# Kernel tuning notes

Hardware: AMD Instinct MI355X
Metric: run time of the kernel (lower is better)

Reference implementation:

```python
import jax, jax.numpy as jnp
import numpy as np
import math

NEG_INF = -1000000000.0
D_EMBED = 1024
D_K = 1024
N_HEADS = 16
D_H = D_EMBED // N_HEADS


def setup_inputs() -> dict:
    key = jax.random.key(0)
    ks = jax.random.split(key, 12)
    B, S = 2, 2048
    s = 0.02
    return {
        "embed": jax.random.normal(ks[0], (B, S, D_EMBED), dtype=jnp.float32),
        "key": jax.random.normal(ks[1], (B, S, D_K), dtype=jnp.float32),
        "attn_mask": jax.random.randint(ks[2], (B, S, S), 0, 2, dtype=jnp.int32),
        "Wq": jax.random.normal(ks[3], (D_EMBED, D_EMBED), dtype=jnp.float32) * s,
        "bq": jnp.zeros((D_EMBED,), dtype=jnp.float32),
        "Wk": jax.random.normal(ks[4], (D_EMBED, D_K), dtype=jnp.float32) * s,
        "bk": jnp.zeros((D_EMBED,), dtype=jnp.float32),
        "Wv": jax.random.normal(ks[5], (D_EMBED, D_K), dtype=jnp.float32) * s,
        "bv": jnp.zeros((D_EMBED,), dtype=jnp.float32),
        "Wo": jax.random.normal(ks[6], (D_EMBED, D_EMBED), dtype=jnp.float32) * s,
        "bo": jnp.zeros((D_EMBED,), dtype=jnp.float32),
    }


def _alibi_bias(seq_len: int, n_heads: int) -> jnp.ndarray:
    # symmetric |i-j| distances, slopes 2^-(8k/H) for k=1..H
    r = jnp.arange(seq_len)
    pos = jnp.abs(r[None, :] - r[:, None]).astype(jnp.float32)  # [S, S]
    step = 8.0 / n_heads
    ms = 2.0 ** (-jnp.arange(step, 8.0 + step, step, dtype=jnp.float32))  # [H]
    return ms[:, None, None] * pos[None, :, :]  # [H, S, S]


def reference(embed, key, attn_mask, Wq, bq, Wk, bk, Wv, bv, Wo, bo):
    B, Sq, _ = embed.shape
    Sk = key.shape[1]
    Q = embed @ Wq.T + bq          # [B, Sq, D]
    K = key @ Wk.T + bk            # [B, Sk, D]
    V = key @ Wv.T + bv            # [B, Sk, D]
    Qh = Q.reshape(B, Sq, N_HEADS, D_H).transpose(0, 2, 1, 3)  # [B, H, Sq, d_h]
    Kh = K.reshape(B, Sk, N_HEADS, D_H).transpose(0, 2, 1, 3)
    Vh = V.reshape(B, Sk, N_HEADS, D_H).transpose(0, 2, 1, 3)
    attn = jnp.einsum("bhqd,bhkd->bhqk", Qh, Kh)
    # ALiBi bias subtracted BEFORE scaling (as in source)
    attn = attn - _alibi_bias(Sq, N_HEADS)[None]
    attn = attn * (1.0 / math.sqrt(D_EMBED))  # note: scale uses d_embed, not d_h
    attn = jnp.where(attn_mask[:, None, :, :] == 0, NEG_INF, attn)
    attn = jax.nn.softmax(attn, axis=-1)
    out = jnp.einsum("bhqk,bhkd->bhqd", attn, Vh)
    out = out.transpose(0, 2, 1, 3).reshape(B, Sq, D_EMBED)
    return out @ Wo.T + bo
```

## Files before the change

### kernel.cpp

```cpp
#include <hip/hip_runtime.h>


typedef _Float16 f16;
typedef __attribute__((ext_vector_type(8))) _Float16 f16x8;
typedef __attribute__((ext_vector_type(4))) _Float16 f16x4;
typedef __attribute__((ext_vector_type(4))) float f32x4;
typedef unsigned long long u64;
typedef unsigned int u32;

#define MFMA16 __builtin_amdgcn_mfma_f32_16x16x32_f16
#define MFMA16K16 __builtin_amdgcn_mfma_f32_16x16x16f16

__device__ __forceinline__ void gl16(const f16* g, f16* l) {
    __builtin_amdgcn_global_load_lds(
        (const __attribute__((address_space(1))) void*)(const void*)g,
        (__attribute__((address_space(3))) void*)(void*)l,
        16, 0, 0);
}

__global__ __launch_bounds__(256) void k_convert(
    const float* __restrict__ embed, const float* __restrict__ key,
    const float* __restrict__ wq, const float* __restrict__ wk,
    const float* __restrict__ wv, const float* __restrict__ wo,
    f16* __restrict__ xe, f16* __restrict__ xk,
    f16* __restrict__ wqh, f16* __restrict__ wkh,
    f16* __restrict__ wvh, f16* __restrict__ woh)
{
    long g = (long)blockIdx.x * 256 + threadIdx.x;
    const float* src; f16* dst; long off;
    if (g < 524288)       { src = embed; dst = xe; off = g; }
    else if (g < 1048576) { src = key;   dst = xk; off = g - 524288; }
    else {
        long t = g - 1048576; int wi = (int)(t >> 17); off = t & 131071;
        if (wi == 0)      { src = wq; dst = wqh; }
        else if (wi == 1) { src = wk; dst = wkh; }
        else if (wi == 2) { src = wv; dst = wvh; }
        else              { src = wo; dst = woh; }
    }
    const float4* s4 = (const float4*)src;
    float4 a = s4[off * 2], b = s4[off * 2 + 1];
    f16x8 o;
    o[0]=(f16)a.x; o[1]=(f16)a.y; o[2]=(f16)a.z; o[3]=(f16)a.w;
    o[4]=(f16)b.x; o[5]=(f16)b.y; o[6]=(f16)b.z; o[7]=(f16)b.w;
    *(f16x8*)(dst + off * 8) = o;
}

__global__ __launch_bounds__(256) void k_packmask(
    const int* __restrict__ mask, u64* __restrict__ bits)
{
    int gw = (blockIdx.x * 256 + threadIdx.x) >> 6;
    int lane = threadIdx.x & 63;
    const int* row = mask + (long)gw * 2048;
    u64* out = bits + (long)gw * 32;
    #pragma unroll 4
    for (int c = 0; c < 32; ++c) {
        int v = row[c * 64 + lane];
        u64 b = __ballot(v != 0);
        if (lane == 0) out[c] = b;
    }
}

__global__ __launch_bounds__(256) void k_qkv(
    const f16* __restrict__ xe, const f16* __restrict__ xk,
    const f16* __restrict__ wqh, const f16* __restrict__ wkh, const f16* __restrict__ wvh,
    const float* __restrict__ bq, const float* __restrict__ bk, const float* __restrict__ bv,
    f16* __restrict__ Qh, f16* __restrict__ Kh, f16* __restrict__ Vt)
{
    int bid = blockIdx.x;
    int which = bid >> 8;
    int rr_ = bid & 255;
    int tm = rr_ >> 3, tn = rr_ & 7;
    const f16* X = (which == 0) ? xe : xk;
    const f16* W = (which == 0) ? wqh : (which == 1) ? wkh : wvh;
    const float* bias = (which == 0) ? bq : (which == 1) ? bk : bv;

    __shared__ f16 smem[128 * 136];
    f16* la = smem;
    f16* lb = smem + 128 * 64;

    int tid = threadIdx.x;
    int lane = tid & 63, wid = tid >> 6;
    int wr = wid >> 1, wc = wid & 1;
    int lm = lane & 15, qd = lane >> 4;

    f32x4 acc[4][4];
    #pragma unroll
    for (int i = 0; i < 4; i++)
        #pragma unroll
        for (int j = 0; j < 4; j++) acc[i][j] = (f32x4)0.0f;

    int m0 = tm * 128, n0 = tn * 128;

    for (int kt = 0; kt < 16; ++kt) {
        int k0 = kt * 64;
        __syncthreads();
        #pragma unroll
        for (int t = 0; t < 4; ++t) {
            int cid = tid + t * 256;
            int row = cid >> 3;
            int cg = cid & 7;
            int sw = cg ^ (row & 7);
            *(f16x8*)&la[row * 64 + sw * 8] =
                *(const f16x8*)&X[(long)(m0 + row) * 1024 + k0 + cg * 8];
            *(f16x8*)&lb[row * 64 + sw * 8] =
                *(const f16x8*)&W[(long)(n0 + row) * 1024 + k0 + cg * 8];
        }
        __syncthreads();
        #pragma unroll
        for (int ks = 0; ks < 2; ++ks) {
            f16x8 af[4], bfr[4];
            #pragma unroll
            for (int i = 0; i < 4; i++) {
                int m = 64 * wr + 16 * i + lm;
                int g = (ks * 4 + qd) ^ (m & 7);
                af[i] = *(const f16x8*)&la[m * 64 + g * 8];
                int n = 64 * wc + 16 * i + lm;
                int g2 = (ks * 4 + qd) ^ (n & 7);
                bfr[i] = *(const f16x8*)&lb[n * 64 + g2 * 8];
            }
            __builtin_amdgcn_s_setprio(1);
            #pragma unroll
            for (int i = 0; i < 4; i++)
                #pragma unroll
                for (int j = 0; j < 4; j++)
                    acc[i][j] = MFMA16(af[i], bfr[j], acc[i][j], 0, 0, 0);
            __builtin_amdgcn_s_setprio(0);
        }
    }

    if (which == 2) {
        #pragma unroll
        for (int j = 0; j < 4; j++) {
            int n = n0 + 64 * wc + 16 * j + lm;
            float bb = bias[n];
            int h = n >> 6, d = n & 63;
            #pragma unroll
            for (int i = 0; i < 4; i++) {
                int mbase = m0 + 64 * wr + 16 * i + 4 * qd;
                f16x4 pk;
                #pragma unroll
                for (int r = 0; r < 4; ++r) pk[r] = (f16)(acc[i][j][r] + bb);
                int b = mbase >> 11, s = mbase & 2047;
                *(f16x4*)&Vt[(((long)(b * 16 + h)) * 64 + d) * 2048 + s] = pk;
            }
        }
    } else {
        f16* dst = (which == 0) ? Qh : Kh;
        float sc = (which == 0) ? 0.0450842252f : 1.0f;
        __syncthreads();
        #pragma unroll
        for (int j = 0; j < 4; j++) {
            int col = 64 * wc + 16 * j + lm;
            float bb = bias[n0 + col];
            #pragma unroll
            for (int i = 0; i < 4; i++) {
                int row = 64 * wr + 16 * i + 4 * qd;
                #pragma unroll
                for (int r = 0; r < 4; ++r)
                    smem[(row + r) * 136 + col] = (f16)((acc[i][j][r] + bb) * sc);
            }
        }
        __syncthreads();
        #pragma unroll
        for (int t = 0; t < 8; ++t) {
            int ci = tid + t * 256;
            int row = ci >> 4, cg = ci & 15;
            f16x8 v = *(const f16x8*)&smem[row * 136 + cg * 8];
            int m = m0 + row;
            int b = m >> 11, s = m & 2047;
            int h = (n0 >> 6) + (cg >> 3);
            int d0 = (cg & 7) * 8;
            *(f16x8*)&dst[(((long)(b * 16 + h)) * 2048 + s) * 64 + d0] = v;
        }
    }
}

__global__ __launch_bounds__(512, 4) void k_attn(
    const f16* __restrict__ Qh, const f16* __restrict__ Kh, const f16* __restrict__ Vt,
    const u64* __restrict__ mbits, f16* __restrict__ O)
{
    int bid0 = blockIdx.x;
    int bid = (bid0 & 7) * 64 + (bid0 >> 3);
    int qt = bid & 15;
    int h = (bid >> 4) & 15;
    int b = bid >> 8;
    int q0 = qt * 128;

    const f16* Qg = Qh + ((long)(b * 16 + h)) * 2048 * 64;
    const f16* Kg = Kh + ((long)(b * 16 + h)) * 2048 * 64;
    const f16* Vg = Vt + ((long)(b * 16 + h)) * 64 * 2048;

    __shared__ f16 smem[32768];

    int tid = threadIdx.x, lane = tid & 63, wid = tid >> 6;
    int lm = lane & 15, qd = lane >> 4;
    int qs = wid & 3;
    int hf = wid >> 2;

    int qb = q0 + 32 * qs;
    const u64* Mrow0 = mbits + ((long)(b * 2048) + qb + lm) * 32;
    const u64* Mrow1 = Mrow0 + 16 * 32;

    int bi = wid >> 1, sub = wid & 1;
    int rowL = lane >> 3;
    int cgL = (lane & 7) ^ rowL;
    const f16* gsrc; long lstep, istep; int doff;
    if (bi < 2) {
        gsrc = Kg + ((long)(bi * 1024 + sub * 32 + rowL)) * 64 + cgL * 8;
        lstep = 512;
        istep = 4096;
        doff = bi * 4096 + sub * 2048;
    } else {
        int vh = bi - 2;
        gsrc = Vg + ((long)(sub * 32 + rowL)) * 2048 + vh * 1024 + cgL * 8;
        lstep = 16384;
        istep = 64;
        doff = 8192 + vh * 4096 + sub * 2048;
    }

    #define ATTN_STAGE(pb, it)                                                 \
        {                                                                      \
            f16* d0 = smem + (pb) * 16384 + doff;                              \
            const f16* s0_ = gsrc + (it) * istep;                              \
            _Pragma("unroll")                                                  \
            for (int li = 0; li < 4; ++li)                                     \
                gl16(s0_ + li * lstep, d0 + li * 512);                         \
        }

    f16x8 aq[2][2];
    #pragma unroll
    for (int g = 0; g < 2; ++g)
        #pragma unroll
        for (int ksi = 0; ksi < 2; ++ksi)
            aq[g][ksi] = *(const f16x8*)&Qg[(long)(qb + 16 * g + lm) * 64 + ksi * 32 + qd * 8];

    f32x4 oacc[2][4], lacc[2];
    #pragma unroll
    for (int g = 0; g < 2; ++g) {
        #pragma unroll
        for (int c = 0; c < 4; c++) oacc[g][c] = (f32x4)0.0f;
        lacc[g] = (f32x4)0.0f;
    }
    f16x4 vone4;
    #pragma unroll
    for (int j = 0; j < 4; j++) vone4[j] = (f16)1.0f;

    float negc2 = -__builtin_amdgcn_exp2f(-0.5f * (float)(h + 1)) * 0.0450842252f;

    int vgq = qd >> 1;
    int off4 = (qd & 1) * 4;

    ATTN_STAGE(0, 0);
    __syncthreads();

    for (int it = 0; it < 16; ++it) {
        int pb = it & 1;
        if (it < 15) ATTN_STAGE(pb ^ 1, it + 1);

        const f16* ksH = smem + pb * 16384 + hf * 4096;
        const f16* vsH = smem + pb * 16384 + 8192 + hf * 4096;

        u64 wa = Mrow0[hf * 16 + it];
        u64 wb = Mrow1[hf * 16 + it];
        float qmk0 = (float)(qb + lm - hf * 1024 - it * 64 - 4 * qd);
        float qmk1 = qmk0 + 16.0f;

        #pragma unroll
        for (int c = 0; c < 4; ++c) {
            int kr = 16 * c + lm;
            f32x4 s0 = (f32x4)0.0f, s1 = (f32x4)0.0f;
            __builtin_amdgcn_s_setprio(1);
            #pragma unroll
            for (int ksi = 0; ksi < 2; ++ksi) {
                int gg = (ksi * 4 + qd) ^ (kr & 7);
                f16x8 ak = *(const f16x8*)&ksH[kr * 64 + gg * 8];
                s0 = MFMA16(ak, aq[0][ksi], s0, 0, 0, 0);
                s1 = MFMA16(ak, aq[1][ksi], s1, 0, 0, 0);
            }
            __builtin_amdgcn_s_setprio(0);
            u32 niba = (u32)(wa >> (16 * c + 4 * qd)) & 15u;
            u32 nibb = (u32)(wb >> (16 * c + 4 * qd)) & 15u;
            float qc0 = qmk0 - 16.0f * (float)c;
            float qc1 = qmk1 - 16.0f * (float)c;
            f16x4 pk0, pk1;
            #pragma unroll
            for (int r = 0; r < 4; ++r) {
                float u0 = fmaf(fabsf(qc0 - (float)r), negc2, s0[r]);
                u0 = ((niba >> r) & 1u) ? u0 : -1e30f;
                pk0[r] = (f16)__builtin_amdgcn_exp2f(u0);
                float u1 = fmaf(fabsf(qc1 - (float)r), negc2, s1[r]);
                u1 = ((nibb >> r) & 1u) ? u1 : -1e30f;
                pk1[r] = (f16)__builtin_amdgcn_exp2f(u1);
            }
            int vgc = 2 * c + vgq;
            __builtin_amdgcn_s_setprio(1);
            #pragma unroll
            for (int cc = 0; cc < 4; ++cc) {
                int d = 16 * cc + lm;
                f16x4 vb = *(const f16x4*)&vsH[d * 64 + (vgc ^ (d & 7)) * 8 + off4];
                oacc[0][cc] = MFMA16K16(pk0, vb, oacc[0][cc], 0, 0, 0);
                oacc[1][cc] = MFMA16K16(pk1, vb, oacc[1][cc], 0, 0, 0);
            }
            lacc[0] = MFMA16K16(pk0, vone4, lacc[0], 0, 0, 0);
            lacc[1] = MFMA16K16(pk1, vone4, lacc[1], 0, 0, 0);
            __builtin_amdgcn_s_setprio(0);
        }
        __syncthreads();
    }
    #undef ATTN_STAGE

    float* cO = (float*)smem;
    float* lL = (float*)(smem + 16384);
    f16*  fO  = smem + 16640;

    if (hf == 1) {
        #pragma unroll
        for (int g = 0; g < 2; ++g) {
            #pragma unroll
            for (int cc = 0; cc < 4; ++cc)
                #pragma unroll
                for (int r = 0; r < 4; ++r)
                    cO[(qs * 32 + 16 * g + 4 * qd + r) * 64 + 16 * cc + lm] = oacc[g][cc][r];
            if (lm == 0) {
                #pragma unroll
                for (int r = 0; r < 4; ++r)
                    lL[qs * 32 + 16 * g + 4 * qd + r] = lacc[g][r];
            }
        }
    }
    __syncthreads();
    if (hf == 0) {
        #pragma unroll
        for (int g = 0; g < 2; ++g) {
            float linv[4];
            #pragma unroll
            for (int r = 0; r < 4; ++r)
                linv[r] = 1.0f / fmaxf(lacc[g][r] + lL[qs * 32 + 16 * g + 4 * qd + r], 1e-30f);
            #pragma unroll
            for (int cc = 0; cc < 4; ++cc)
                #pragma unroll
                for (int r = 0; r < 4; ++r) {
                    int idx = (qs * 32 + 16 * g + 4 * qd + r) * 64 + 16 * cc + lm;
                    fO[idx] = (f16)((oacc[g][cc][r] + cO[idx]) * linv[r]);
                }
        }
    }
    __syncthreads();
    #pragma unroll
    for (int t = 0; t < 2; ++t) {
        int ci = tid + t * 512;
        int q = ci >> 3, dc = ci & 7;
        f16x8 v = *(const f16x8*)&fO[q * 64 + dc * 8];
        *(f16x8*)&O[((long)(b * 2048 + q0 + q)) * 1024 + h * 64 + dc * 8] = v;
    }
}

__global__ __launch_bounds__(256) void k_proj(
    const f16* __restrict__ Oh, const f16* __restrict__ woh,
    const float* __restrict__ bo, float* __restrict__ out)
{
    int bid = blockIdx.x;
    int tm = bid >> 3, tn = bid & 7;

    __shared__ f16 la[128 * 64];
    __shared__ f16 lb[128 * 64];

    int tid = threadIdx.x;
    int lane = tid & 63, wid = tid >> 6;
    int wr = wid >> 1, wc = wid & 1;
    int lm = lane & 15, qd = lane >> 4;

    f32x4 acc[4][4];
    #pragma unroll
    for (int i = 0; i < 4; i++)
        #pragma unroll
        for (int j = 0; j < 4; j++) acc[i][j] = (f32x4)0.0f;

    int m0 = tm * 128, n0 = tn * 128;

    for (int kt = 0; kt < 16; ++kt) {
        int k0 = kt * 64;
        __syncthreads();
        #pragma unroll
        for (int t = 0; t < 4; ++t) {
            int cid = tid + t * 256;
            int row = cid >> 3;
            int cg = cid & 7;
            int sw = cg ^ (row & 7);
            *(f16x8*)&la[row * 64 + sw * 8] =
                *(const f16x8*)&Oh[(long)(m0 + row) * 1024 + k0 + cg * 8];
            *(f16x8*)&lb[row * 64 + sw * 8] =
                *(const f16x8*)&woh[(long)(n0 + row) * 1024 + k0 + cg * 8];
        }
        __syncthreads();
        #pragma unroll
        for (int ks = 0; ks < 2; ++ks) {
            f16x8 af[4], bfr[4];
            #pragma unroll
            for (int i = 0; i < 4; i++) {
                int m = 64 * wr + 16 * i + lm;
                int g = (ks * 4 + qd) ^ (m & 7);
                af[i] = *(const f16x8*)&la[m * 64 + g * 8];
                int n = 64 * wc + 16 * i + lm;
                int g2 = (ks * 4 + qd) ^ (n & 7);
                bfr[i] = *(const f16x8*)&lb[n * 64 + g2 * 8];
            }
            __builtin_amdgcn_s_setprio(1);
            #pragma unroll
            for (int i = 0; i < 4; i++)
                #pragma unroll
                for (int j = 0; j < 4; j++)
                    acc[i][j] = MFMA16(af[i], bfr[j], acc[i][j], 0, 0, 0);
            __builtin_amdgcn_s_setprio(0);
        }
    }

    #pragma unroll
    for (int j = 0; j < 4; j++) {
        int n = n0 + 64 * wc + 16 * j + lm;
        float bb = bo[n];
        #pragma unroll
        for (int i = 0; i < 4; i++) {
            int mbase = m0 + 64 * wr + 16 * i + 4 * qd;
            #pragma unroll
            for (int r = 0; r < 4; ++r)
                out[(long)(mbase + r) * 1024 + n] = acc[i][j][r] + bb;
        }
    }
}

extern "C" void kernel_launch(void* const* d_in, const int* in_sizes, int n_in,
                              void* d_out, int out_size, void* d_ws, size_t ws_size,
                              hipStream_t stream)
{
    const float* embed = (const float*)d_in[0];
    const float* key   = (const float*)d_in[1];
    const int*   mask  = (const int*)d_in[2];
    const float* Wq = (const float*)d_in[3];
    const float* bq = (const float*)d_in[4];
    const float* Wk = (const float*)d_in[5];
    const float* bk = (const float*)d_in[6];
    const float* Wv = (const float*)d_in[7];
    const float* bv = (const float*)d_in[8];
    const float* Wo = (const float*)d_in[9];
    const float* bo = (const float*)d_in[10];

    char* ws = (char*)d_ws;
    f16* xe  = (f16*)(ws + 0);
    f16* xk  = (f16*)(ws + 8388608);
    f16* wqh = (f16*)(ws + 16777216);
    f16* wkh = (f16*)(ws + 18874368);
    f16* wvh = (f16*)(ws + 20971520);
    f16* woh = (f16*)(ws + 23068672);
    f16* Qh  = (f16*)(ws + 25165824);
    f16* Kh  = (f16*)(ws + 33554432);
    f16* Vt  = (f16*)(ws + 41943040);
    f16* Oh  = (f16*)(ws + 50331648);
    u64* mb  = (u64*)(ws + 58720256);
    float* out = (float*)d_out;

    k_convert<<<6144, 256, 0, stream>>>(embed, key, Wq, Wk, Wv, Wo,
                                        xe, xk, wqh, wkh, wvh, woh);
    k_packmask<<<1024, 256, 0, stream>>>(mask, mb);
    k_qkv<<<768, 256, 0, stream>>>(xe, xk, wqh, wkh, wvh, bq, bk, bv, Qh, Kh, Vt);
    k_attn<<<512, 512, 0, stream>>>(Qh, Kh, Vt, mb, Oh);
    k_proj<<<256, 256, 0, stream>>>(Oh, woh, bo, out);
}
```

Baseline: 277.1 us.

## Double-buffer QKV and output-projection GEMMs with register prefetch and XCD-aware block remap

Both GEMM kernels move from single-buffered 64-wide K tiles to double-buffered 32-wide K tiles. The next tile is prefetched into registers while MFMAs run on the current LDS buffer, which overlaps global loads with compute. Block indices are also remapped in strides of 8 so that consecutive blocks placed on the same XCD share operand tiles for L2 reuse. The cost is twice as many loop iterations and barriers per K, plus extra registers for the prefetched data.

Measured after the change: 263.3 us. 5.0% less time.

```diff
diff --git a/kernel.cpp b/kernel.cpp
--- a/kernel.cpp
+++ b/kernel.cpp
@@ -66,7 +66,8 @@
     const float* __restrict__ bq, const float* __restrict__ bk, const float* __restrict__ bv,
     f16* __restrict__ Qh, f16* __restrict__ Kh, f16* __restrict__ Vt)
 {
-    int bid = blockIdx.x;
+    int bid0 = blockIdx.x;
+    int bid = (bid0 & 7) * 96 + (bid0 >> 3);
     int which = bid >> 8;
     int rr_ = bid & 255;
     int tm = rr_ >> 3, tn = rr_ & 7;
@@ -74,9 +75,7 @@
     const f16* W = (which == 0) ? wqh : (which == 1) ? wkh : wvh;
     const float* bias = (which == 0) ? bq : (which == 1) ? bk : bv;
 
-    __shared__ f16 smem[128 * 136];
-    f16* la = smem;
-    f16* lb = smem + 128 * 64;
+    __shared__ f16 smem[17408];
 
     int tid = threadIdx.x;
     int lane = tid & 63, wid = tid >> 6;
@@ -91,40 +90,59 @@
 
     int m0 = tm * 128, n0 = tn * 128;
 
-    for (int kt = 0; kt < 16; ++kt) {
-        int k0 = kt * 64;
+    int row0 = tid >> 2, cg0 = tid & 3;
+    int row1 = (tid + 256) >> 2, cg1 = (tid + 256) & 3;
+    int lw0 = row0 * 32 + (cg0 ^ (row0 & 3)) * 8;
+    int lw1 = row1 * 32 + (cg1 ^ (row1 & 3)) * 8;
+    const f16* gx0 = X + (long)(m0 + row0) * 1024 + cg0 * 8;
+    const f16* gx1 = X + (long)(m0 + row1) * 1024 + cg1 * 8;
+    const f16* gw0 = W + (long)(n0 + row0) * 1024 + cg0 * 8;
+    const f16* gw1 = W + (long)(n0 + row1) * 1024 + cg1 * 8;
+
+    f16x8 rx0, rx1, rw0, rw1;
+    rx0 = *(const f16x8*)&gx0[0];
+    rx1 = *(const f16x8*)&gx1[0];
+    rw0 = *(const f16x8*)&gw0[0];
+    rw1 = *(const f16x8*)&gw1[0];
+    *(f16x8*)&smem[lw0] = rx0;
+    *(f16x8*)&smem[lw1] = rx1;
+    *(f16x8*)&smem[4096 + lw0] = rw0;
+    *(f16x8*)&smem[4096 + lw1] = rw1;
+
+    for (int kt = 0; kt < 32; ++kt) {
+        int pb = kt & 1;
         __syncthreads();
-        #pragma unroll
-        for (int t = 0; t < 4; ++t) {
-            int cid = tid + t * 256;
-            int row = cid >> 3;
-            int cg = cid & 7;
-            int sw = cg ^ (row & 7);
-            *(f16x8*)&la[row * 64 + sw * 8] =
-                *(const f16x8*)&X[(long)(m0 + row) * 1024 + k0 + cg * 8];
-            *(f16x8*)&lb[row * 64 + sw * 8] =
-                *(const f16x8*)&W[(long)(n0 + row) * 1024 + k0 + cg * 8];
-        }
+        if (kt < 31) {
+            int k0 = (kt + 1) * 32;
+            rx0 = *(const f16x8*)&gx0[k0];
+            rx1 = *(const f16x8*)&gx1[k0];
+            rw0 = *(const f16x8*)&gw0[k0];
+            rw1 = *(const f16x8*)&gw1[k0];
+        }
+        const f16* la = smem + pb * 8192;
+        const f16* lb = la + 4096;
+        f16x8 af[4], bfr[4];
+        #pragma unroll
+        for (int i = 0; i < 4; i++) {
+            int m = 64 * wr + 16 * i + lm;
+            af[i] = *(const f16x8*)&la[m * 32 + (qd ^ (m & 3)) * 8];
+            int n = 64 * wc + 16 * i + lm;
+            bfr[i] = *(const f16x8*)&lb[n * 32 + (qd ^ (n & 3)) * 8];
+        }
+        __builtin_amdgcn_s_setprio(1);
+        #pragma unroll
+        for (int i = 0; i < 4; i++)
+            #pragma unroll
+            for (int j = 0; j < 4; j++)
+                acc[i][j] = MFMA16(af[i], bfr[j], acc[i][j], 0, 0, 0);
+        __builtin_amdgcn_s_setprio(0);
         __syncthreads();
-        #pragma unroll
-        for (int ks = 0; ks < 2; ++ks) {
-            f16x8 af[4], bfr[4];
-            #pragma unroll
-            for (int i = 0; i < 4; i++) {
-                int m = 64 * wr + 16 * i + lm;
-                int g = (ks * 4 + qd) ^ (m & 7);
-                af[i] = *(const f16x8*)&la[m * 64 + g * 8];
-                int n = 64 * wc + 16 * i + lm;
-                int g2 = (ks * 4 + qd) ^ (n & 7);
-                bfr[i] = *(const f16x8*)&lb[n * 64 + g2 * 8];
-            }
-            __builtin_amdgcn_s_setprio(1);
-            #pragma unroll
-            for (int i = 0; i < 4; i++)
-                #pragma unroll
-                for (int j = 0; j < 4; j++)
-                    acc[i][j] = MFMA16(af[i], bfr[j], acc[i][j], 0, 0, 0);
-            __builtin_amdgcn_s_setprio(0);
+        if (kt < 31) {
+            f16* d = smem + (pb ^ 1) * 8192;
+            *(f16x8*)&d[lw0] = rx0;
+            *(f16x8*)&d[lw1] = rx1;
+            *(f16x8*)&d[4096 + lw0] = rw0;
+            *(f16x8*)&d[4096 + lw1] = rw1;
         }
     }
 
@@ -147,7 +165,6 @@
     } else {
         f16* dst = (which == 0) ? Qh : Kh;
         float sc = (which == 0) ? 0.0450842252f : 1.0f;
-        __syncthreads();
         #pragma unroll
         for (int j = 0; j < 4; j++) {
             int col = 64 * wc + 16 * j + lm;
@@ -359,11 +376,11 @@
     const f16* __restrict__ Oh, const f16* __restrict__ woh,
     const float* __restrict__ bo, float* __restrict__ out)
 {
-    int bid = blockIdx.x;
+    int bid0 = blockIdx.x;
+    int bid = (bid0 & 7) * 32 + (bid0 >> 3);
     int tm = bid >> 3, tn = bid & 7;
 
-    __shared__ f16 la[128 * 64];
-    __shared__ f16 lb[128 * 64];
+    __shared__ f16 smem[16384];
 
     int tid = threadIdx.x;
     int lane = tid & 63, wid = tid >> 6;
@@ -378,40 +395,59 @@
 
     int m0 = tm * 128, n0 = tn * 128;
 
-    for (int kt = 0; kt < 16; ++kt) {
-        int k0 = kt * 64;
+    int row0 = tid >> 2, cg0 = tid & 3;
+    int row1 = (tid + 256) >> 2, cg1 = (tid + 256) & 3;
+    int lw0 = row0 * 32 + (cg0 ^ (row0 & 3)) * 8;
+    int lw1 = row1 * 32 + (cg1 ^ (row1 & 3)) * 8;
+    const f16* gx0 = Oh  + (long)(m0 + row0) * 1024 + cg0 * 8;
+    const f16* gx1 = Oh  + (long)(m0 + row1) * 1024 + cg1 * 8;
+    const f16* gw0 = woh + (long)(n0 + row0) * 1024 + cg0 * 8;
+    const f16* gw1 = woh + (long)(n0 + row1) * 1024 + cg1 * 8;
+
+    f16x8 rx0, rx1, rw0, rw1;
+    rx0 = *(const f16x8*)&gx0[0];
+    rx1 = *(const f16x8*)&gx1[0];
+    rw0 = *(const f16x8*)&gw0[0];
+    rw1 = *(const f16x8*)&gw1[0];
+    *(f16x8*)&smem[lw0] = rx0;
+    *(f16x8*)&smem[lw1] = rx1;
+    *(f16x8*)&smem[4096 + lw0] = rw0;
+    *(f16x8*)&smem[4096 + lw1] = rw1;
+
+    for (int kt = 0; kt < 32; ++kt) {
+        int pb = kt & 1;
         __syncthreads();
-        #pragma unroll
-        for (int t = 0; t < 4; ++t) {
-            int cid = tid + t * 256;
-            int row = cid >> 3;
-            int cg = cid & 7;
-            int sw = cg ^ (row & 7);
-            *(f16x8*)&la[row * 64 + sw * 8] =
-                *(const f16x8*)&Oh[(long)(m0 + row) * 1024 + k0 + cg * 8];
-            *(f16x8*)&lb[row * 64 + sw * 8] =
-                *(const f16x8*)&woh[(long)(n0 + row) * 1024 + k0 + cg * 8];
-        }
+        if (kt < 31) {
+            int k0 = (kt + 1) * 32;
+            rx0 = *(const f16x8*)&gx0[k0];
+            rx1 = *(const f16x8*)&gx1[k0];
+            rw0 = *(const f16x8*)&gw0[k0];
+            rw1 = *(const f16x8*)&gw1[k0];
+        }
+        const f16* la = smem + pb * 8192;
+        const f16* lb = la + 4096;
+        f16x8 af[4], bfr[4];
+        #pragma unroll
+        for (int i = 0; i < 4; i++) {
+            int m = 64 * wr + 16 * i + lm;
+            af[i] = *(const f16x8*)&la[m * 32 + (qd ^ (m & 3)) * 8];
+            int n = 64 * wc + 16 * i + lm;
+            bfr[i] = *(const f16x8*)&lb[n * 32 + (qd ^ (n & 3)) * 8];
+        }
+        __builtin_amdgcn_s_setprio(1);
+        #pragma unroll
+        for (int i = 0; i < 4; i++)
+            #pragma unroll
+            for (int j = 0; j < 4; j++)
+                acc[i][j] = MFMA16(af[i], bfr[j], acc[i][j], 0, 0, 0);
+        __builtin_amdgcn_s_setprio(0);
         __syncthreads();
-        #pragma unroll
-        for (int ks = 0; ks < 2; ++ks) {
-            f16x8 af[4], bfr[4];
-            #pragma unroll
-            for (int i = 0; i < 4; i++) {
-                int m = 64 * wr + 16 * i + lm;
-                int g = (ks * 4 + qd) ^ (m & 7);
-                af[i] = *(const f16x8*)&la[m * 64 + g * 8];
-                int n = 64 * wc + 16 * i + lm;
-                int g2 = (ks * 4 + qd) ^ (n & 7);
-                bfr[i] = *(const f16x8*)&lb[n * 64 + g2 * 8];
-            }
-            __builtin_amdgcn_s_setprio(1);
-            #pragma unroll
-            for (int i = 0; i < 4; i++)
-                #pragma unroll
-                for (int j = 0; j < 4; j++)
-                    acc[i][j] = MFMA16(af[i], bfr[j], acc[i][j], 0, 0, 0);
-            __builtin_amdgcn_s_setprio(0);
+        if (kt < 31) {
+            f16* d = smem + (pb ^ 1) * 8192;
+            *(f16x8*)&d[lw0] = rx0;
+            *(f16x8*)&d[lw1] = rx1;
+            *(f16x8*)&d[4096 + lw0] = rw0;
+            *(f16x8*)&d[4096 + lw1] = rw1;
         }
     }
 
```
